# Optimization experiments

Measured on AMD Instinct MI355X. Metric: run time of the kernel, lower is better.

Reference implementation:

```python
import jax, jax.numpy as jnp
import numpy as np

N = 256
FEAT = 1024           # box_head.fc7.out_features
HID_REL = 256         # RelationProposalNetwork hidden_dim
GCN_HID = 256         # gcn_hidden
HEADS = 4
NUM_PARTS = 20
OUT = NUM_PARTS + 1
TOPK = 3
IN_GCN = FEAT + 4


def setup_inputs() -> dict:
    key = jax.random.key(0)
    ks = jax.random.split(key, 16)
    features = jax.random.normal(ks[0], (N, FEAT), jnp.float32)
    # valid pixel-space boxes (x1, y1, x2, y2) inside an 800x800 image
    xy = jax.random.uniform(ks[1], (N, 2), jnp.float32, 0.0, 700.0)
    wh = jax.random.uniform(ks[2], (N, 2), jnp.float32, 8.0, 100.0)
    boxes = jnp.concatenate([xy, xy + wh], axis=1)
    s = 0.02
    W_fc1 = jax.random.normal(ks[3], (2 * FEAT + 4, HID_REL), jnp.float32) * s
    b_fc1 = jnp.zeros((HID_REL,), jnp.float32)
    W_fc2 = jax.random.normal(ks[4], (HID_REL, 1), jnp.float32) * s
    b_fc2 = jnp.zeros((1,), jnp.float32)
    W1 = jax.random.normal(ks[5], (IN_GCN, HEADS * GCN_HID), jnp.float32) * s
    a_src1 = jax.random.normal(ks[6], (HEADS, GCN_HID), jnp.float32) * s
    a_dst1 = jax.random.normal(ks[7], (HEADS, GCN_HID), jnp.float32) * s
    b1 = jnp.zeros((HEADS * GCN_HID,), jnp.float32)
    W2 = jax.random.normal(ks[8], (HEADS * GCN_HID, OUT), jnp.float32) * s
    a_src2 = jax.random.normal(ks[9], (1, OUT), jnp.float32) * s
    a_dst2 = jax.random.normal(ks[10], (1, OUT), jnp.float32) * s
    b2 = jnp.zeros((OUT,), jnp.float32)
    return {
        "features": features, "boxes": boxes,
        "W_fc1": W_fc1, "b_fc1": b_fc1, "W_fc2": W_fc2, "b_fc2": b_fc2,
        "W1": W1, "a_src1": a_src1, "a_dst1": a_dst1, "b1": b1,
        "W2": W2, "a_src2": a_src2, "a_dst2": a_dst2, "b2": b2,
        "img_h": 800, "img_w": 800,
    }


def _gat_layer(x, W, a_src, a_dst, bias, s, t, n, heads, ch):
    # PyG GATConv: message flows edge_index[0] (s) -> edge_index[1] (t),
    # softmax over incoming edges of each target node t.
    h = (x @ W).reshape(n, heads, ch)                       # [n, H, C]
    e = jax.nn.leaky_relu(
        jnp.einsum("ehc,hc->eh", h[s], a_src)
        + jnp.einsum("ehc,hc->eh", h[t], a_dst), 0.2)        # [E, H]
    m = jnp.full((n, heads), -1e30, e.dtype).at[t].max(e)    # segment max
    p = jnp.exp(e - m[t])
    denom = jax.ops.segment_sum(p, t, num_segments=n)
    alpha = p / denom[t]                                     # [E, H]
    out = jax.ops.segment_sum(alpha[:, :, None] * h[s], t, num_segments=n)
    return out.reshape(n, heads * ch) + bias


def _forward(features, boxes, W_fc1, b_fc1, W_fc2, b_fc2,
             W1, a_src1, a_dst1, b1, W2, a_src2, a_dst2, b2, img_h, img_w):
    n = features.shape[0]
    # --- RelationProposalNetwork: dense O(N^2) pairwise MLP ---
    f1 = jnp.broadcast_to(features[:, None, :], (n, n, FEAT))
    f2 = jnp.broadcast_to(features[None, :, :], (n, n, FEAT))
    geom = jnp.abs(boxes[:, None, :] - boxes[None, :, :])    # [n, n, 4]
    pair = jnp.concatenate([f1, f2, geom], axis=-1)          # [n, n, 2052]
    hid = jax.nn.relu(pair @ W_fc1 + b_fc1)                  # [n, n, 256]
    rel = (hid @ W_fc2 + b_fc2)[..., 0]                      # [n, n]
    # --- top-k graph construction (drop first = self, as in source) ---
    idx = jax.lax.top_k(rel, TOPK + 1)[1][:, 1:]             # [n, topk]
    s_e = jnp.repeat(jnp.arange(n), TOPK)                    # edge_index[0]
    t_e = idx.reshape(-1)                                    # edge_index[1]
    loops = jnp.arange(n)                                    # GATConv add_self_loops
    s_e = jnp.concatenate([s_e, loops])
    t_e = jnp.concatenate([t_e, loops])
    # --- normalized box geometry node features ---
    scale = jnp.array([img_w, img_h, img_w, img_h], jnp.float32)
    nb = boxes / scale
    geomn = jnp.stack([nb[:, 0], nb[:, 1], nb[:, 2] - nb[:, 0], nb[:, 3] - nb[:, 1]], axis=1)
    gcn_in = jnp.concatenate([features, geomn], axis=1)      # [n, 1028]
    # --- AttentionalGCN: GAT(heads=4) -> ReLU -> GAT(heads=1) ---
    h1 = jax.nn.relu(_gat_layer(gcn_in, W1, a_src1, a_dst1, b1, s_e, t_e, n, HEADS, GCN_HID))
    logits = _gat_layer(h1, W2, a_src2, a_dst2, b2, s_e, t_e, n, 1, OUT)
    return logits


def reference(features, boxes, W_fc1, b_fc1, W_fc2, b_fc2,
              W1, a_src1, a_dst1, b1, W2, a_src2, a_dst2, b2, img_h, img_w):
    logits = _forward(features, boxes, W_fc1, b_fc1, W_fc2, b_fc2,
                      W1, a_src1, a_dst1, b1, W2, a_src2, a_dst2, b2, img_h, img_w)
    labels = jnp.argmax(logits, axis=1)
    return logits, labels
```

## Files before the change

### kernel.cpp

```cpp
#include <hip/hip_runtime.h>
#include <math.h>

#define NN 256
#define FEAT 1024
#define HIDR 256
#define HEADS 4
#define GCNH 256
#define M1 1024
#define OUTC 21
#define MAXDEG (NN + 1)
#define KC 8
#define KCH (FEAT / KC)
#define FCOLS 1536

__global__ __launch_bounds__(256) void k_big(
        const float* __restrict__ feat, const float* __restrict__ Wfc1,
        const float* __restrict__ W1, float* __restrict__ P) {
    __shared__ float fS[8][KCH];
    int rg = blockIdx.x, cg = blockIdx.y, kc = blockIdx.z;
    int tid = threadIdx.x;
    int r0 = rg * 8, k0 = kc * KCH;
    for (int x = tid; x < 8 * KCH; x += 256) {
        int r = x >> 7, kk = x & (KCH - 1);
        fS[r][kk] = feat[(size_t)(r0 + r) * FEAT + k0 + kk];
    }
    __syncthreads();
    int gc = cg * 512 + tid * 2;
    const float* pW;
    int ld;
    if (gc < 256)      { pW = Wfc1 + (size_t)k0 * HIDR + gc;                  ld = HIDR; }
    else if (gc < 512) { pW = Wfc1 + (size_t)(FEAT + k0) * HIDR + (gc - 256); ld = HIDR; }
    else               { pW = W1   + (size_t)k0 * M1 + (gc - 512);            ld = M1;   }
    float2 acc[8];
#pragma unroll
    for (int r = 0; r < 8; r++) { acc[r].x = 0.f; acc[r].y = 0.f; }
    float2 w0 = *(const float2*)(pW);
    float2 w1 = *(const float2*)(pW + ld);
    float2 w2 = *(const float2*)(pW + 2 * ld);
    float2 w3 = *(const float2*)(pW + 3 * ld);
    for (int kk = 0; kk < KCH; kk += 4) {
        pW += 4 * ld;
        float2 n0 = *(const float2*)(pW);
        float2 n1 = *(const float2*)(pW + ld);
        float2 n2 = *(const float2*)(pW + 2 * ld);
        float2 n3 = *(const float2*)(pW + 3 * ld);
#pragma unroll
        for (int r = 0; r < 8; r++) {
            float4 f = *(const float4*)&fS[r][kk];
            acc[r].x = fmaf(f.x, w0.x, acc[r].x); acc[r].y = fmaf(f.x, w0.y, acc[r].y);
            acc[r].x = fmaf(f.y, w1.x, acc[r].x); acc[r].y = fmaf(f.y, w1.y, acc[r].y);
            acc[r].x = fmaf(f.z, w2.x, acc[r].x); acc[r].y = fmaf(f.z, w2.y, acc[r].y);
            acc[r].x = fmaf(f.w, w3.x, acc[r].x); acc[r].y = fmaf(f.w, w3.y, acc[r].y);
        }
        w0 = n0; w1 = n1; w2 = n2; w3 = n3;
    }
    float* Pp = P + ((size_t)kc * NN + r0) * FCOLS + gc;
#pragma unroll
    for (int r = 0; r < 8; r++)
        *(float2*)(Pp + (size_t)r * FCOLS) = acc[r];
}

__global__ __launch_bounds__(384) void k_redfix(
        const float* __restrict__ P, const float* __restrict__ bfc1,
        const float* __restrict__ boxes, const int* __restrict__ imh,
        const int* __restrict__ imw, const float* __restrict__ W1,
        const float* __restrict__ as1, const float* __restrict__ ad1,
        float* __restrict__ A, float* __restrict__ BT4,
        float* __restrict__ hpre, float* __restrict__ es1,
        float* __restrict__ ed1, float* __restrict__ geomn) {
    __shared__ float gS[4];
    int row = blockIdx.x, tid = threadIdx.x;
    int c4 = tid * 4;
    const float* p = P + (size_t)row * FCOLS + c4;
    const size_t str = (size_t)NN * FCOLS;
    float4 t0 = *(const float4*)(p);
    float4 t1 = *(const float4*)(p + str);
    float4 t2 = *(const float4*)(p + 2 * str);
    float4 t3 = *(const float4*)(p + 3 * str);
    float4 t4 = *(const float4*)(p + 4 * str);
    float4 t5 = *(const float4*)(p + 5 * str);
    float4 t6 = *(const float4*)(p + 6 * str);
    float4 t7 = *(const float4*)(p + 7 * str);
    float4 s;
    s.x = ((t0.x + t1.x) + (t2.x + t3.x)) + ((t4.x + t5.x) + (t6.x + t7.x));
    s.y = ((t0.y + t1.y) + (t2.y + t3.y)) + ((t4.y + t5.y) + (t6.y + t7.y));
    s.z = ((t0.z + t1.z) + (t2.z + t3.z)) + ((t4.z + t5.z) + (t6.z + t7.z));
    s.w = ((t0.w + t1.w) + (t2.w + t3.w)) + ((t4.w + t5.w) + (t6.w + t7.w));
    if (tid == 0) {
        float w = (float)imw[0], h = (float)imh[0];
        float x1 = boxes[row * 4 + 0] / w, y1 = boxes[row * 4 + 1] / h;
        float x2 = boxes[row * 4 + 2] / w, y2 = boxes[row * 4 + 3] / h;
        gS[0] = x1; gS[1] = y1; gS[2] = x2 - x1; gS[3] = y2 - y1;
        geomn[row * 4 + 0] = x1;
        geomn[row * 4 + 1] = y1;
        geomn[row * 4 + 2] = x2 - x1;
        geomn[row * 4 + 3] = y2 - y1;
    }
    __syncthreads();
    if (c4 < 256) {
        float4 b = *(const float4*)(bfc1 + c4);
        s.x += b.x; s.y += b.y; s.z += b.z; s.w += b.w;
        *(float4*)(A + (size_t)row * HIDR + c4) = s;
    } else if (c4 < 512) {
        int kk = c4 - 256;
        *(float4*)(BT4 + (size_t)(kk >> 2) * (NN * 4) + row * 4) = s;
    } else {
        int ch = c4 - 512;
        float g0 = gS[0], g1 = gS[1], g2 = gS[2], g3 = gS[3];
        float4 wv;
        wv = *(const float4*)(W1 + (size_t)(FEAT + 0) * M1 + ch);
        s.x = fmaf(g0, wv.x, s.x); s.y = fmaf(g0, wv.y, s.y);
        s.z = fmaf(g0, wv.z, s.z); s.w = fmaf(g0, wv.w, s.w);
        wv = *(const float4*)(W1 + (size_t)(FEAT + 1) * M1 + ch);
        s.x = fmaf(g1, wv.x, s.x); s.y = fmaf(g1, wv.y, s.y);
        s.z = fmaf(g1, wv.z, s.z); s.w = fmaf(g1, wv.w, s.w);
        wv = *(const float4*)(W1 + (size_t)(FEAT + 2) * M1 + ch);
        s.x = fmaf(g2, wv.x, s.x); s.y = fmaf(g2, wv.y, s.y);
        s.z = fmaf(g2, wv.z, s.z); s.w = fmaf(g2, wv.w, s.w);
        wv = *(const float4*)(W1 + (size_t)(FEAT + 3) * M1 + ch);
        s.x = fmaf(g3, wv.x, s.x); s.y = fmaf(g3, wv.y, s.y);
        s.z = fmaf(g3, wv.z, s.z); s.w = fmaf(g3, wv.w, s.w);
        *(float4*)(hpre + (size_t)row * M1 + ch) = s;
        float4 a = *(const float4*)(as1 + ch);
        float4 b = *(const float4*)(ad1 + ch);
        float ps = s.x * a.x + s.y * a.y + s.z * a.z + s.w * a.w;
        float pd = s.x * b.x + s.y * b.y + s.z * b.z + s.w * b.w;
#pragma unroll
        for (int o = 32; o > 0; o >>= 1) {
            ps += __shfl_down(ps, o);
            pd += __shfl_down(pd, o);
        }
        if ((tid & 63) == 0) {
            int head = (tid - 128) >> 6;
            es1[row * 4 + head] = ps;
            ed1[row * 4 + head] = pd;
        }
    }
}

__global__ __launch_bounds__(512) void k_reltopk(
        const float* __restrict__ A, const float* __restrict__ BT4,
        const float* __restrict__ boxes, const float* __restrict__ Wfc1,
        const float* __restrict__ Wfc2, int* __restrict__ idxTop) {
    __shared__ float As[HIDR], w2s[HIDR], wg0[HIDR], wg1[HIDR], wg2[HIDR], wg3[HIDR];
    __shared__ float sval[512];
    __shared__ unsigned long long swk[8];
    __shared__ int win;
    int i = blockIdx.x, tid = threadIdx.x;
    int j = tid & 255, half = tid >> 8;
    if (tid < 256) {
        As[tid]  = A[i * HIDR + tid];
        w2s[tid] = Wfc2[tid];
        wg0[tid] = Wfc1[(size_t)(2 * FEAT + 0) * HIDR + tid];
    } else {
        int q = tid - 256;
        wg1[q] = Wfc1[(size_t)(2 * FEAT + 1) * HIDR + q];
        wg2[q] = Wfc1[(size_t)(2 * FEAT + 2) * HIDR + q];
        wg3[q] = Wfc1[(size_t)(2 * FEAT + 3) * HIDR + q];
    }
    float bi0 = boxes[i * 4 + 0], bi1 = boxes[i * 4 + 1];
    float bi2 = boxes[i * 4 + 2], bi3 = boxes[i * 4 + 3];
    float g0 = fabsf(bi0 - boxes[j * 4 + 0]);
    float g1 = fabsf(bi1 - boxes[j * 4 + 1]);
    float g2 = fabsf(bi2 - boxes[j * 4 + 2]);
    float g3 = fabsf(bi3 - boxes[j * 4 + 3]);
    __syncthreads();
    int k0 = half * 128;
    const float* pB = BT4 + (size_t)(k0 >> 2) * (NN * 4) + j * 4;
    float acc = 0.f;
    for (int kk = k0; kk < k0 + 128; kk += 4) {
        float4 a4 = *(const float4*)&As[kk];
        float4 w4 = *(const float4*)&w2s[kk];
        float4 q0 = *(const float4*)&wg0[kk];
        float4 q1 = *(const float4*)&wg1[kk];
        float4 q2 = *(const float4*)&wg2[kk];
        float4 q3 = *(const float4*)&wg3[kk];
        float4 b4 = *(const float4*)pB;
        pB += NN * 4;
        float v;
        v = a4.x + b4.x; v = fmaf(g0, q0.x, v); v = fmaf(g1, q1.x, v);
        v = fmaf(g2, q2.x, v); v = fmaf(g3, q3.x, v);
        acc = fmaf(fmaxf(v, 0.f), w4.x, acc);
        v = a4.y + b4.y; v = fmaf(g0, q0.y, v); v = fmaf(g1, q1.y, v);
        v = fmaf(g2, q2.y, v); v = fmaf(g3, q3.y, v);
        acc = fmaf(fmaxf(v, 0.f), w4.y, acc);
        v = a4.z + b4.z; v = fmaf(g0, q0.z, v); v = fmaf(g1, q1.z, v);
        v = fmaf(g2, q2.z, v); v = fmaf(g3, q3.z, v);
        acc = fmaf(fmaxf(v, 0.f), w4.z, acc);
        v = a4.w + b4.w; v = fmaf(g0, q0.w, v); v = fmaf(g1, q1.w, v);
        v = fmaf(g2, q2.w, v); v = fmaf(g3, q3.w, v);
        acc = fmaf(fmaxf(v, 0.f), w4.w, acc);
    }
    sval[tid] = acc;
    __syncthreads();
    if (tid < 256) sval[tid] = sval[tid] + sval[tid + 256];
    __syncthreads();
    for (int r = 0; r < 4; r++) {
        unsigned long long key = 0ULL;
        if (tid < 256) {
            unsigned u = __float_as_uint(sval[tid]);
            u = (u & 0x80000000u) ? ~u : (u | 0x80000000u);
            key = ((unsigned long long)u << 32) | (unsigned)(NN - 1 - tid);
        }
#pragma unroll
        for (int o = 32; o > 0; o >>= 1) {
            unsigned long long nk = __shfl_down(key, o);
            if (nk > key) key = nk;
        }
        if ((tid & 63) == 0) swk[tid >> 6] = key;
        __syncthreads();
        if (tid == 0) {
            unsigned long long m = swk[0];
#pragma unroll
            for (int q = 1; q < 8; q++) if (swk[q] > m) m = swk[q];
            int wj = NN - 1 - (int)(m & 0xFFFFFFFFu);
            win = wj;
            if (r > 0) idxTop[i * 3 + (r - 1)] = wj;
        }
        __syncthreads();
        if (tid == win) sval[tid] = -1e38f;
        __syncthreads();
    }
}

__global__ __launch_bounds__(256) void k_gat1h2(
        const float* __restrict__ idxTopF, const float* __restrict__ hpre,
        const float* __restrict__ es1, const float* __restrict__ ed1,
        const float* __restrict__ b1, const float* __restrict__ W2,
        const float* __restrict__ as2, const float* __restrict__ ad2,
        int* __restrict__ deg, int* __restrict__ inlist,
        float* __restrict__ h2, float* __restrict__ es2,
        float* __restrict__ ed2) {
    const int* idxTop = (const int*)idxTopF;
    __shared__ int pfx[NN];
    __shared__ int lst[MAXDEG];
    __shared__ int dgS;
    __shared__ float sc[MAXDEG * 4];
    __shared__ float mh[4], dh[4];
    __shared__ float sh[M1];
    __shared__ float part[12 * OUTC];
    __shared__ float h2row[OUTC];
    int t = blockIdx.x, tid = threadIdx.x;
    int f = (idxTop[tid * 3 + 0] == t) | (idxTop[tid * 3 + 1] == t)
          | (idxTop[tid * 3 + 2] == t);
    pfx[tid] = f;
    __syncthreads();
    for (int o = 1; o < NN; o <<= 1) {
        int add = (tid >= o) ? pfx[tid - o] : 0;
        __syncthreads();
        pfx[tid] += add;
        __syncthreads();
    }
    if (f) {
        lst[pfx[tid] - 1] = tid;
        inlist[t * MAXDEG + (pfx[tid] - 1)] = tid;
    }
    if (tid == NN - 1) {
        int d = pfx[NN - 1];
        lst[d] = t;
        inlist[t * MAXDEG + d] = t;
        dgS = d + 1;
        deg[t] = d + 1;
    }
    __syncthreads();
    int dg = dgS;
    for (int p = tid; p < dg * 4; p += 256) {
        int e = p >> 2, h = p & 3;
        int s = lst[e];
        float v = es1[s * 4 + h] + ed1[t * 4 + h];
        sc[p] = v >= 0.f ? v : 0.2f * v;
    }
    __syncthreads();
    if (tid < 4) {
        float m = -1e30f;
        for (int e = 0; e < dg; e++) m = fmaxf(m, sc[e * 4 + tid]);
        float s = 0.f;
        for (int e = 0; e < dg; e++) s += expf(sc[e * 4 + tid] - m);
        mh[tid] = m; dh[tid] = s;
    }
    __syncthreads();
    for (int p = tid; p < dg * 4; p += 256) {
        int h = p & 3;
        sc[p] = expf(sc[p] - mh[h]) / dh[h];
    }
    __syncthreads();
    float acc[4] = {0.f, 0.f, 0.f, 0.f};
    for (int e = 0; e < dg; e++) {
        int s = lst[e];
        const float* hs = hpre + (size_t)s * M1;
#pragma unroll
        for (int q = 0; q < 4; q++)
            acc[q] = fmaf(sc[e * 4 + q], hs[q * GCNH + tid], acc[q]);
    }
#pragma unroll
    for (int q = 0; q < 4; q++) {
        int c = q * GCNH + tid;
        sh[c] = fmaxf(acc[q] + b1[c], 0.f);
    }
    __syncthreads();
    if (tid < 252) {
        int o = tid % OUTC, p = tid / OUTC;
        float a2 = 0.f;
        for (int d = p; d < M1; d += 12)
            a2 = fmaf(sh[d], W2[d * OUTC + o], a2);
        part[p * OUTC + o] = a2;
    }
    __syncthreads();
    if (tid < OUTC) {
        float s = 0.f;
        for (int p = 0; p < 12; p++) s += part[p * OUTC + tid];
        h2[t * OUTC + tid] = s;
        h2row[tid] = s;
    }
    __syncthreads();
    if (tid == 0) {
        float s = 0.f, dd = 0.f;
        for (int k = 0; k < OUTC; k++) {
            s = fmaf(h2row[k], as2[k], s);
            dd = fmaf(h2row[k], ad2[k], dd);
        }
        es2[t] = s; ed2[t] = dd;
    }
}

__global__ __launch_bounds__(64) void k_gat2(
        const float* __restrict__ h2, const float* __restrict__ es2,
        const float* __restrict__ ed2, const int* __restrict__ deg,
        const int* __restrict__ inlist, const float* __restrict__ b2,
        float* __restrict__ out) {
    __shared__ float sc[MAXDEG];
    __shared__ float md[2];
    __shared__ float lv[OUTC];
    int t = blockIdx.x, tid = threadIdx.x;
    int dg = deg[t];
    float edt = ed2[t];
    for (int p = tid; p < dg; p += 64) {
        int s = inlist[t * MAXDEG + p];
        float v = es2[s] + edt;
        sc[p] = v >= 0.f ? v : 0.2f * v;
    }
    __syncthreads();
    if (tid == 0) {
        float m = -1e30f;
        for (int e = 0; e < dg; e++) m = fmaxf(m, sc[e]);
        float s = 0.f;
        for (int e = 0; e < dg; e++) s += expf(sc[e] - m);
        md[0] = m; md[1] = s;
    }
    __syncthreads();
    if (tid < OUTC) {
        float acc = 0.f;
        for (int e = 0; e < dg; e++) {
            int s = inlist[t * MAXDEG + e];
            float a = expf(sc[e] - md[0]) / md[1];
            acc = fmaf(a, h2[s * OUTC + tid], acc);
        }
        float v = acc + b2[tid];
        out[t * OUTC + tid] = v;
        lv[tid] = v;
    }
    __syncthreads();
    if (tid == 0) {
        int best = 0;
        float bv = lv[0];
        for (int o = 1; o < OUTC; o++)
            if (lv[o] > bv) { bv = lv[o]; best = o; }
        out[NN * OUTC + t] = (float)best;
    }
}

extern "C" void kernel_launch(void* const* d_in, const int* in_sizes, int n_in,
                              void* d_out, int out_size, void* d_ws,
                              size_t ws_size, hipStream_t stream) {
    const float* feat  = (const float*)d_in[0];
    const float* boxes = (const float*)d_in[1];
    const float* Wfc1  = (const float*)d_in[2];
    const float* bfc1  = (const float*)d_in[3];
    const float* Wfc2  = (const float*)d_in[4];
    const float* bfc2  = (const float*)d_in[5];   (void)bfc2;
    const float* W1    = (const float*)d_in[6];
    const float* as1   = (const float*)d_in[7];
    const float* ad1   = (const float*)d_in[8];
    const float* b1    = (const float*)d_in[9];
    const float* W2    = (const float*)d_in[10];
    const float* as2   = (const float*)d_in[11];
    const float* ad2   = (const float*)d_in[12];
    const float* b2    = (const float*)d_in[13];
    const int*   imh   = (const int*)d_in[14];
    const int*   imw   = (const int*)d_in[15];

    float* ws = (float*)d_ws;
    float* P     = ws;  ws += KC * NN * FCOLS;
    float* A     = ws;  ws += NN * HIDR;
    float* BT4   = ws;  ws += NN * HIDR;
    float* hpre  = ws;  ws += NN * M1;
    float* es1   = ws;  ws += NN * 4;
    float* ed1   = ws;  ws += NN * 4;
    float* h2    = ws;  ws += NN * OUTC;
    float* es2   = ws;  ws += NN;
    float* ed2   = ws;  ws += NN;
    float* geomn = ws;  ws += NN * 4;
    int* deg     = (int*)ws;
    int* inlist  = deg + NN;
    int* idxTop  = inlist + NN * MAXDEG;

    float* out = (float*)d_out;

    k_big<<<dim3(32, 3, KC), 256, 0, stream>>>(feat, Wfc1, W1, P);
    k_redfix<<<NN, 384, 0, stream>>>(P, bfc1, boxes, imh, imw, W1, as1, ad1,
                                     A, BT4, hpre, es1, ed1, geomn);
    k_reltopk<<<NN, 512, 0, stream>>>(A, BT4, boxes, Wfc1, Wfc2, idxTop);
    k_gat1h2<<<NN, 256, 0, stream>>>((const float*)idxTop, hpre, es1, ed1,
                                     b1, W2, as2, ad2, deg, inlist,
                                     h2, es2, ed2);
    k_gat2<<<NN, 64, 0, stream>>>(h2, es2, ed2, deg, inlist, b2, out);
}
```

Measured before the change: 163.2 us.

## Fuse tail kernels into one cooperative kernel with grid syncs; retile big GEMM

Merges the reduction/fixup, relation top-k, GAT layer 1 and GAT layer 2 kernels into a single cooperative kernel of 256 blocks x 512 threads. The stages are separated by grid.sync(), and the A matrix stays in shared memory instead of going through global memory. This removes three kernel launches and their gaps. The front GEMM is also retiled to 16 rows per block with 16 K-chunks, which adds more partial sums to reduce. Grid-wide barriers have their own cost, and the larger per-block register and LDS footprint could limit co-residency.

```diff
diff --git a/kernel.cpp b/kernel.cpp
--- a/kernel.cpp
+++ b/kernel.cpp
@@ -1,5 +1,8 @@
 #include <hip/hip_runtime.h>
+#include <hip/hip_cooperative_groups.h>
 #include <math.h>
+
+namespace coopg = cooperative_groups;
 
 #define NN 256
 #define FEAT 1024
@@ -9,31 +12,32 @@
 #define M1 1024
 #define OUTC 21
 #define MAXDEG (NN + 1)
-#define KC 8
+#define KC 16
 #define KCH (FEAT / KC)
+#define RB 16
 #define FCOLS 1536
 
 __global__ __launch_bounds__(256) void k_big(
         const float* __restrict__ feat, const float* __restrict__ Wfc1,
         const float* __restrict__ W1, float* __restrict__ P) {
-    __shared__ float fS[8][KCH];
-    int rg = blockIdx.x, cg = blockIdx.y, kc = blockIdx.z;
+    __shared__ float fS[RB][KCH];
+    int rg = blockIdx.x, cgy = blockIdx.y, kc = blockIdx.z;
     int tid = threadIdx.x;
-    int r0 = rg * 8, k0 = kc * KCH;
-    for (int x = tid; x < 8 * KCH; x += 256) {
-        int r = x >> 7, kk = x & (KCH - 1);
+    int r0 = rg * RB, k0 = kc * KCH;
+    for (int x = tid; x < RB * KCH; x += 256) {
+        int r = x >> 6, kk = x & (KCH - 1);
         fS[r][kk] = feat[(size_t)(r0 + r) * FEAT + k0 + kk];
     }
     __syncthreads();
-    int gc = cg * 512 + tid * 2;
+    int gc = cgy * 512 + tid * 2;
     const float* pW;
     int ld;
     if (gc < 256)      { pW = Wfc1 + (size_t)k0 * HIDR + gc;                  ld = HIDR; }
     else if (gc < 512) { pW = Wfc1 + (size_t)(FEAT + k0) * HIDR + (gc - 256); ld = HIDR; }
     else               { pW = W1   + (size_t)k0 * M1 + (gc - 512);            ld = M1;   }
-    float2 acc[8];
-#pragma unroll
-    for (int r = 0; r < 8; r++) { acc[r].x = 0.f; acc[r].y = 0.f; }
+    float2 acc[RB];
+#pragma unroll
+    for (int r = 0; r < RB; r++) { acc[r].x = 0.f; acc[r].y = 0.f; }
     float2 w0 = *(const float2*)(pW);
     float2 w1 = *(const float2*)(pW + ld);
     float2 w2 = *(const float2*)(pW + 2 * ld);
@@ -45,7 +49,7 @@
         float2 n2 = *(const float2*)(pW + 2 * ld);
         float2 n3 = *(const float2*)(pW + 3 * ld);
 #pragma unroll
-        for (int r = 0; r < 8; r++) {
+        for (int r = 0; r < RB; r++) {
             float4 f = *(const float4*)&fS[r][kk];
             acc[r].x = fmaf(f.x, w0.x, acc[r].x); acc[r].y = fmaf(f.x, w0.y, acc[r].y);
             acc[r].x = fmaf(f.y, w1.x, acc[r].x); acc[r].y = fmaf(f.y, w1.y, acc[r].y);
@@ -56,316 +60,323 @@
     }
     float* Pp = P + ((size_t)kc * NN + r0) * FCOLS + gc;
 #pragma unroll
-    for (int r = 0; r < 8; r++)
+    for (int r = 0; r < RB; r++)
         *(float2*)(Pp + (size_t)r * FCOLS) = acc[r];
 }
 
-__global__ __launch_bounds__(384) void k_redfix(
+__global__ __launch_bounds__(512) void k_tail(
         const float* __restrict__ P, const float* __restrict__ bfc1,
         const float* __restrict__ boxes, const int* __restrict__ imh,
         const int* __restrict__ imw, const float* __restrict__ W1,
         const float* __restrict__ as1, const float* __restrict__ ad1,
-        float* __restrict__ A, float* __restrict__ BT4,
+        const float* __restrict__ Wfc1, const float* __restrict__ Wfc2,
+        const float* __restrict__ b1, const float* __restrict__ W2,
+        const float* __restrict__ as2, const float* __restrict__ ad2,
+        const float* __restrict__ b2, float* __restrict__ BT4,
         float* __restrict__ hpre, float* __restrict__ es1,
-        float* __restrict__ ed1, float* __restrict__ geomn) {
+        float* __restrict__ ed1, int* __restrict__ idxTop,
+        int* __restrict__ deg, int* __restrict__ inlist,
+        float* __restrict__ h2, float* __restrict__ es2,
+        float* __restrict__ ed2, float* __restrict__ out) {
+    coopg::grid_group grid = coopg::this_grid();
     __shared__ float gS[4];
-    int row = blockIdx.x, tid = threadIdx.x;
-    int c4 = tid * 4;
-    const float* p = P + (size_t)row * FCOLS + c4;
-    const size_t str = (size_t)NN * FCOLS;
-    float4 t0 = *(const float4*)(p);
-    float4 t1 = *(const float4*)(p + str);
-    float4 t2 = *(const float4*)(p + 2 * str);
-    float4 t3 = *(const float4*)(p + 3 * str);
-    float4 t4 = *(const float4*)(p + 4 * str);
-    float4 t5 = *(const float4*)(p + 5 * str);
-    float4 t6 = *(const float4*)(p + 6 * str);
-    float4 t7 = *(const float4*)(p + 7 * str);
-    float4 s;
-    s.x = ((t0.x + t1.x) + (t2.x + t3.x)) + ((t4.x + t5.x) + (t6.x + t7.x));
-    s.y = ((t0.y + t1.y) + (t2.y + t3.y)) + ((t4.y + t5.y) + (t6.y + t7.y));
-    s.z = ((t0.z + t1.z) + (t2.z + t3.z)) + ((t4.z + t5.z) + (t6.z + t7.z));
-    s.w = ((t0.w + t1.w) + (t2.w + t3.w)) + ((t4.w + t5.w) + (t6.w + t7.w));
-    if (tid == 0) {
-        float w = (float)imw[0], h = (float)imh[0];
-        float x1 = boxes[row * 4 + 0] / w, y1 = boxes[row * 4 + 1] / h;
-        float x2 = boxes[row * 4 + 2] / w, y2 = boxes[row * 4 + 3] / h;
-        gS[0] = x1; gS[1] = y1; gS[2] = x2 - x1; gS[3] = y2 - y1;
-        geomn[row * 4 + 0] = x1;
-        geomn[row * 4 + 1] = y1;
-        geomn[row * 4 + 2] = x2 - x1;
-        geomn[row * 4 + 3] = y2 - y1;
-    }
-    __syncthreads();
-    if (c4 < 256) {
-        float4 b = *(const float4*)(bfc1 + c4);
-        s.x += b.x; s.y += b.y; s.z += b.z; s.w += b.w;
-        *(float4*)(A + (size_t)row * HIDR + c4) = s;
-    } else if (c4 < 512) {
-        int kk = c4 - 256;
-        *(float4*)(BT4 + (size_t)(kk >> 2) * (NN * 4) + row * 4) = s;
-    } else {
-        int ch = c4 - 512;
-        float g0 = gS[0], g1 = gS[1], g2 = gS[2], g3 = gS[3];
-        float4 wv;
-        wv = *(const float4*)(W1 + (size_t)(FEAT + 0) * M1 + ch);
-        s.x = fmaf(g0, wv.x, s.x); s.y = fmaf(g0, wv.y, s.y);
-        s.z = fmaf(g0, wv.z, s.z); s.w = fmaf(g0, wv.w, s.w);
-        wv = *(const float4*)(W1 + (size_t)(FEAT + 1) * M1 + ch);
-        s.x = fmaf(g1, wv.x, s.x); s.y = fmaf(g1, wv.y, s.y);
-        s.z = fmaf(g1, wv.z, s.z); s.w = fmaf(g1, wv.w, s.w);
-        wv = *(const float4*)(W1 + (size_t)(FEAT + 2) * M1 + ch);
-        s.x = fmaf(g2, wv.x, s.x); s.y = fmaf(g2, wv.y, s.y);
-        s.z = fmaf(g2, wv.z, s.z); s.w = fmaf(g2, wv.w, s.w);
-        wv = *(const float4*)(W1 + (size_t)(FEAT + 3) * M1 + ch);
-        s.x = fmaf(g3, wv.x, s.x); s.y = fmaf(g3, wv.y, s.y);
-        s.z = fmaf(g3, wv.z, s.z); s.w = fmaf(g3, wv.w, s.w);
-        *(float4*)(hpre + (size_t)row * M1 + ch) = s;
-        float4 a = *(const float4*)(as1 + ch);
-        float4 b = *(const float4*)(ad1 + ch);
-        float ps = s.x * a.x + s.y * a.y + s.z * a.z + s.w * a.w;
-        float pd = s.x * b.x + s.y * b.y + s.z * b.z + s.w * b.w;
-#pragma unroll
-        for (int o = 32; o > 0; o >>= 1) {
-            ps += __shfl_down(ps, o);
-            pd += __shfl_down(pd, o);
-        }
-        if ((tid & 63) == 0) {
-            int head = (tid - 128) >> 6;
-            es1[row * 4 + head] = ps;
-            ed1[row * 4 + head] = pd;
-        }
-    }
-}
-
-__global__ __launch_bounds__(512) void k_reltopk(
-        const float* __restrict__ A, const float* __restrict__ BT4,
-        const float* __restrict__ boxes, const float* __restrict__ Wfc1,
-        const float* __restrict__ Wfc2, int* __restrict__ idxTop) {
-    __shared__ float As[HIDR], w2s[HIDR], wg0[HIDR], wg1[HIDR], wg2[HIDR], wg3[HIDR];
+    __shared__ float As[HIDR], w2s[HIDR];
+    __shared__ float wg0[HIDR], wg1[HIDR], wg2[HIDR], wg3[HIDR];
     __shared__ float sval[512];
     __shared__ unsigned long long swk[8];
     __shared__ int win;
-    int i = blockIdx.x, tid = threadIdx.x;
-    int j = tid & 255, half = tid >> 8;
-    if (tid < 256) {
-        As[tid]  = A[i * HIDR + tid];
-        w2s[tid] = Wfc2[tid];
-        wg0[tid] = Wfc1[(size_t)(2 * FEAT + 0) * HIDR + tid];
-    } else {
-        int q = tid - 256;
-        wg1[q] = Wfc1[(size_t)(2 * FEAT + 1) * HIDR + q];
-        wg2[q] = Wfc1[(size_t)(2 * FEAT + 2) * HIDR + q];
-        wg3[q] = Wfc1[(size_t)(2 * FEAT + 3) * HIDR + q];
-    }
-    float bi0 = boxes[i * 4 + 0], bi1 = boxes[i * 4 + 1];
-    float bi2 = boxes[i * 4 + 2], bi3 = boxes[i * 4 + 3];
-    float g0 = fabsf(bi0 - boxes[j * 4 + 0]);
-    float g1 = fabsf(bi1 - boxes[j * 4 + 1]);
-    float g2 = fabsf(bi2 - boxes[j * 4 + 2]);
-    float g3 = fabsf(bi3 - boxes[j * 4 + 3]);
-    __syncthreads();
-    int k0 = half * 128;
-    const float* pB = BT4 + (size_t)(k0 >> 2) * (NN * 4) + j * 4;
-    float acc = 0.f;
-    for (int kk = k0; kk < k0 + 128; kk += 4) {
-        float4 a4 = *(const float4*)&As[kk];
-        float4 w4 = *(const float4*)&w2s[kk];
-        float4 q0 = *(const float4*)&wg0[kk];
-        float4 q1 = *(const float4*)&wg1[kk];
-        float4 q2 = *(const float4*)&wg2[kk];
-        float4 q3 = *(const float4*)&wg3[kk];
-        float4 b4 = *(const float4*)pB;
-        pB += NN * 4;
-        float v;
-        v = a4.x + b4.x; v = fmaf(g0, q0.x, v); v = fmaf(g1, q1.x, v);
-        v = fmaf(g2, q2.x, v); v = fmaf(g3, q3.x, v);
-        acc = fmaf(fmaxf(v, 0.f), w4.x, acc);
-        v = a4.y + b4.y; v = fmaf(g0, q0.y, v); v = fmaf(g1, q1.y, v);
-        v = fmaf(g2, q2.y, v); v = fmaf(g3, q3.y, v);
-        acc = fmaf(fmaxf(v, 0.f), w4.y, acc);
-        v = a4.z + b4.z; v = fmaf(g0, q0.z, v); v = fmaf(g1, q1.z, v);
-        v = fmaf(g2, q2.z, v); v = fmaf(g3, q3.z, v);
-        acc = fmaf(fmaxf(v, 0.f), w4.z, acc);
-        v = a4.w + b4.w; v = fmaf(g0, q0.w, v); v = fmaf(g1, q1.w, v);
-        v = fmaf(g2, q2.w, v); v = fmaf(g3, q3.w, v);
-        acc = fmaf(fmaxf(v, 0.f), w4.w, acc);
-    }
-    sval[tid] = acc;
-    __syncthreads();
-    if (tid < 256) sval[tid] = sval[tid] + sval[tid + 256];
-    __syncthreads();
-    for (int r = 0; r < 4; r++) {
-        unsigned long long key = 0ULL;
-        if (tid < 256) {
-            unsigned u = __float_as_uint(sval[tid]);
-            u = (u & 0x80000000u) ? ~u : (u | 0x80000000u);
-            key = ((unsigned long long)u << 32) | (unsigned)(NN - 1 - tid);
-        }
-#pragma unroll
-        for (int o = 32; o > 0; o >>= 1) {
-            unsigned long long nk = __shfl_down(key, o);
-            if (nk > key) key = nk;
-        }
-        if ((tid & 63) == 0) swk[tid >> 6] = key;
-        __syncthreads();
-        if (tid == 0) {
-            unsigned long long m = swk[0];
-#pragma unroll
-            for (int q = 1; q < 8; q++) if (swk[q] > m) m = swk[q];
-            int wj = NN - 1 - (int)(m & 0xFFFFFFFFu);
-            win = wj;
-            if (r > 0) idxTop[i * 3 + (r - 1)] = wj;
-        }
-        __syncthreads();
-        if (tid == win) sval[tid] = -1e38f;
-        __syncthreads();
-    }
-}
-
-__global__ __launch_bounds__(256) void k_gat1h2(
-        const float* __restrict__ idxTopF, const float* __restrict__ hpre,
-        const float* __restrict__ es1, const float* __restrict__ ed1,
-        const float* __restrict__ b1, const float* __restrict__ W2,
-        const float* __restrict__ as2, const float* __restrict__ ad2,
-        int* __restrict__ deg, int* __restrict__ inlist,
-        float* __restrict__ h2, float* __restrict__ es2,
-        float* __restrict__ ed2) {
-    const int* idxTop = (const int*)idxTopF;
-    __shared__ int pfx[NN];
+    __shared__ int pfxS[NN];
     __shared__ int lst[MAXDEG];
     __shared__ int dgS;
     __shared__ float sc[MAXDEG * 4];
     __shared__ float mh[4], dh[4];
-    __shared__ float sh[M1];
+    __shared__ float shh[M1];
     __shared__ float part[12 * OUTC];
     __shared__ float h2row[OUTC];
-    int t = blockIdx.x, tid = threadIdx.x;
-    int f = (idxTop[tid * 3 + 0] == t) | (idxTop[tid * 3 + 1] == t)
-          | (idxTop[tid * 3 + 2] == t);
-    pfx[tid] = f;
-    __syncthreads();
-    for (int o = 1; o < NN; o <<= 1) {
-        int add = (tid >= o) ? pfx[tid - o] : 0;
-        __syncthreads();
-        pfx[tid] += add;
-        __syncthreads();
-    }
-    if (f) {
-        lst[pfx[tid] - 1] = tid;
-        inlist[t * MAXDEG + (pfx[tid] - 1)] = tid;
-    }
-    if (tid == NN - 1) {
-        int d = pfx[NN - 1];
-        lst[d] = t;
-        inlist[t * MAXDEG + d] = t;
-        dgS = d + 1;
-        deg[t] = d + 1;
-    }
-    __syncthreads();
-    int dg = dgS;
-    for (int p = tid; p < dg * 4; p += 256) {
-        int e = p >> 2, h = p & 3;
-        int s = lst[e];
-        float v = es1[s * 4 + h] + ed1[t * 4 + h];
-        sc[p] = v >= 0.f ? v : 0.2f * v;
-    }
-    __syncthreads();
-    if (tid < 4) {
-        float m = -1e30f;
-        for (int e = 0; e < dg; e++) m = fmaxf(m, sc[e * 4 + tid]);
-        float s = 0.f;
-        for (int e = 0; e < dg; e++) s += expf(sc[e * 4 + tid] - m);
-        mh[tid] = m; dh[tid] = s;
-    }
-    __syncthreads();
-    for (int p = tid; p < dg * 4; p += 256) {
-        int h = p & 3;
-        sc[p] = expf(sc[p] - mh[h]) / dh[h];
-    }
-    __syncthreads();
-    float acc[4] = {0.f, 0.f, 0.f, 0.f};
-    for (int e = 0; e < dg; e++) {
-        int s = lst[e];
-        const float* hs = hpre + (size_t)s * M1;
-#pragma unroll
-        for (int q = 0; q < 4; q++)
-            acc[q] = fmaf(sc[e * 4 + q], hs[q * GCNH + tid], acc[q]);
-    }
-#pragma unroll
-    for (int q = 0; q < 4; q++) {
-        int c = q * GCNH + tid;
-        sh[c] = fmaxf(acc[q] + b1[c], 0.f);
-    }
-    __syncthreads();
-    if (tid < 252) {
-        int o = tid % OUTC, p = tid / OUTC;
-        float a2 = 0.f;
-        for (int d = p; d < M1; d += 12)
-            a2 = fmaf(sh[d], W2[d * OUTC + o], a2);
-        part[p * OUTC + o] = a2;
-    }
-    __syncthreads();
-    if (tid < OUTC) {
-        float s = 0.f;
-        for (int p = 0; p < 12; p++) s += part[p * OUTC + tid];
-        h2[t * OUTC + tid] = s;
-        h2row[tid] = s;
-    }
-    __syncthreads();
-    if (tid == 0) {
-        float s = 0.f, dd = 0.f;
-        for (int k = 0; k < OUTC; k++) {
-            s = fmaf(h2row[k], as2[k], s);
-            dd = fmaf(h2row[k], ad2[k], dd);
-        }
-        es2[t] = s; ed2[t] = dd;
-    }
-}
-
-__global__ __launch_bounds__(64) void k_gat2(
-        const float* __restrict__ h2, const float* __restrict__ es2,
-        const float* __restrict__ ed2, const int* __restrict__ deg,
-        const int* __restrict__ inlist, const float* __restrict__ b2,
-        float* __restrict__ out) {
-    __shared__ float sc[MAXDEG];
+    __shared__ float sc2[MAXDEG];
     __shared__ float md[2];
     __shared__ float lv[OUTC];
-    int t = blockIdx.x, tid = threadIdx.x;
-    int dg = deg[t];
-    float edt = ed2[t];
-    for (int p = tid; p < dg; p += 64) {
-        int s = inlist[t * MAXDEG + p];
-        float v = es2[s] + edt;
-        sc[p] = v >= 0.f ? v : 0.2f * v;
+
+    const int b = blockIdx.x;
+    const int tid = threadIdx.x;
+
+    if (tid == 0) {
+        float w = (float)imw[0], h = (float)imh[0];
+        float x1 = boxes[b * 4 + 0] / w, y1 = boxes[b * 4 + 1] / h;
+        float x2 = boxes[b * 4 + 2] / w, y2 = boxes[b * 4 + 3] / h;
+        gS[0] = x1; gS[1] = y1; gS[2] = x2 - x1; gS[3] = y2 - y1;
     }
     __syncthreads();
-    if (tid == 0) {
-        float m = -1e30f;
-        for (int e = 0; e < dg; e++) m = fmaxf(m, sc[e]);
-        float s = 0.f;
-        for (int e = 0; e < dg; e++) s += expf(sc[e] - m);
-        md[0] = m; md[1] = s;
-    }
-    __syncthreads();
-    if (tid < OUTC) {
+    if (tid < 384) {
+        int c4 = tid * 4;
+        const float* p = P + (size_t)b * FCOLS + c4;
+        const size_t str = (size_t)NN * FCOLS;
+        float4 a0 = *(const float4*)(p);
+        float4 a1 = *(const float4*)(p + str);
+        float4 a2 = *(const float4*)(p + 2 * str);
+        float4 a3 = *(const float4*)(p + 3 * str);
+#pragma unroll
+        for (int q = 4; q < KC; q += 4) {
+            float4 t0 = *(const float4*)(p + (size_t)q * str);
+            float4 t1 = *(const float4*)(p + (size_t)(q + 1) * str);
+            float4 t2 = *(const float4*)(p + (size_t)(q + 2) * str);
+            float4 t3 = *(const float4*)(p + (size_t)(q + 3) * str);
+            a0.x += t0.x; a0.y += t0.y; a0.z += t0.z; a0.w += t0.w;
+            a1.x += t1.x; a1.y += t1.y; a1.z += t1.z; a1.w += t1.w;
+            a2.x += t2.x; a2.y += t2.y; a2.z += t2.z; a2.w += t2.w;
+            a3.x += t3.x; a3.y += t3.y; a3.z += t3.z; a3.w += t3.w;
+        }
+        float4 s;
+        s.x = (a0.x + a1.x) + (a2.x + a3.x);
+        s.y = (a0.y + a1.y) + (a2.y + a3.y);
+        s.z = (a0.z + a1.z) + (a2.z + a3.z);
+        s.w = (a0.w + a1.w) + (a2.w + a3.w);
+        if (c4 < 256) {
+            float4 bb = *(const float4*)(bfc1 + c4);
+            As[c4 + 0] = s.x + bb.x;
+            As[c4 + 1] = s.y + bb.y;
+            As[c4 + 2] = s.z + bb.z;
+            As[c4 + 3] = s.w + bb.w;
+        } else if (c4 < 512) {
+            int kk = c4 - 256;
+            *(float4*)(BT4 + (size_t)(kk >> 2) * (NN * 4) + b * 4) = s;
+        } else {
+            int ch = c4 - 512;
+            float g0 = gS[0], g1 = gS[1], g2 = gS[2], g3 = gS[3];
+            float4 wv;
+            wv = *(const float4*)(W1 + (size_t)(FEAT + 0) * M1 + ch);
+            s.x = fmaf(g0, wv.x, s.x); s.y = fmaf(g0, wv.y, s.y);
+            s.z = fmaf(g0, wv.z, s.z); s.w = fmaf(g0, wv.w, s.w);
+            wv = *(const float4*)(W1 + (size_t)(FEAT + 1) * M1 + ch);
+            s.x = fmaf(g1, wv.x, s.x); s.y = fmaf(g1, wv.y, s.y);
+            s.z = fmaf(g1, wv.z, s.z); s.w = fmaf(g1, wv.w, s.w);
+            wv = *(const float4*)(W1 + (size_t)(FEAT + 2) * M1 + ch);
+            s.x = fmaf(g2, wv.x, s.x); s.y = fmaf(g2, wv.y, s.y);
+            s.z = fmaf(g2, wv.z, s.z); s.w = fmaf(g2, wv.w, s.w);
+            wv = *(const float4*)(W1 + (size_t)(FEAT + 3) * M1 + ch);
+            s.x = fmaf(g3, wv.x, s.x); s.y = fmaf(g3, wv.y, s.y);
+            s.z = fmaf(g3, wv.z, s.z); s.w = fmaf(g3, wv.w, s.w);
+            *(float4*)(hpre + (size_t)b * M1 + ch) = s;
+            float4 av = *(const float4*)(as1 + ch);
+            float4 dv = *(const float4*)(ad1 + ch);
+            float ps = s.x * av.x + s.y * av.y + s.z * av.z + s.w * av.w;
+            float pd = s.x * dv.x + s.y * dv.y + s.z * dv.z + s.w * dv.w;
+#pragma unroll
+            for (int o = 32; o > 0; o >>= 1) {
+                ps += __shfl_down(ps, o);
+                pd += __shfl_down(pd, o);
+            }
+            if ((tid & 63) == 0) {
+                int head = (tid - 128) >> 6;
+                es1[b * 4 + head] = ps;
+                ed1[b * 4 + head] = pd;
+            }
+        }
+    }
+    grid.sync();
+
+    {
+        int j = tid & 255, half = tid >> 8;
+        if (tid < 256) {
+            w2s[tid] = Wfc2[tid];
+            wg0[tid] = Wfc1[(size_t)(2 * FEAT + 0) * HIDR + tid];
+        } else {
+            int q = tid - 256;
+            wg1[q] = Wfc1[(size_t)(2 * FEAT + 1) * HIDR + q];
+            wg2[q] = Wfc1[(size_t)(2 * FEAT + 2) * HIDR + q];
+            wg3[q] = Wfc1[(size_t)(2 * FEAT + 3) * HIDR + q];
+        }
+        float bi0 = boxes[b * 4 + 0], bi1 = boxes[b * 4 + 1];
+        float bi2 = boxes[b * 4 + 2], bi3 = boxes[b * 4 + 3];
+        float g0 = fabsf(bi0 - boxes[j * 4 + 0]);
+        float g1 = fabsf(bi1 - boxes[j * 4 + 1]);
+        float g2 = fabsf(bi2 - boxes[j * 4 + 2]);
+        float g3 = fabsf(bi3 - boxes[j * 4 + 3]);
+        __syncthreads();
+        int k0 = half * 128;
+        const float* pB = BT4 + (size_t)(k0 >> 2) * (NN * 4) + j * 4;
         float acc = 0.f;
-        for (int e = 0; e < dg; e++) {
-            int s = inlist[t * MAXDEG + e];
-            float a = expf(sc[e] - md[0]) / md[1];
-            acc = fmaf(a, h2[s * OUTC + tid], acc);
-        }
-        float v = acc + b2[tid];
-        out[t * OUTC + tid] = v;
-        lv[tid] = v;
-    }
-    __syncthreads();
-    if (tid == 0) {
-        int best = 0;
-        float bv = lv[0];
-        for (int o = 1; o < OUTC; o++)
-            if (lv[o] > bv) { bv = lv[o]; best = o; }
-        out[NN * OUTC + t] = (float)best;
+        for (int kk = k0; kk < k0 + 128; kk += 4) {
+            float4 a4 = *(const float4*)&As[kk];
+            float4 w4 = *(const float4*)&w2s[kk];
+            float4 q0 = *(const float4*)&wg0[kk];
+            float4 q1 = *(const float4*)&wg1[kk];
+            float4 q2 = *(const float4*)&wg2[kk];
+            float4 q3 = *(const float4*)&wg3[kk];
+            float4 b4 = *(const float4*)pB;
+            pB += NN * 4;
+            float v;
+            v = a4.x + b4.x; v = fmaf(g0, q0.x, v); v = fmaf(g1, q1.x, v);
+            v = fmaf(g2, q2.x, v); v = fmaf(g3, q3.x, v);
+            acc = fmaf(fmaxf(v, 0.f), w4.x, acc);
+            v = a4.y + b4.y; v = fmaf(g0, q0.y, v); v = fmaf(g1, q1.y, v);
+            v = fmaf(g2, q2.y, v); v = fmaf(g3, q3.y, v);
+            acc = fmaf(fmaxf(v, 0.f), w4.y, acc);
+            v = a4.z + b4.z; v = fmaf(g0, q0.z, v); v = fmaf(g1, q1.z, v);
+            v = fmaf(g2, q2.z, v); v = fmaf(g3, q3.z, v);
+            acc = fmaf(fmaxf(v, 0.f), w4.z, acc);
+            v = a4.w + b4.w; v = fmaf(g0, q0.w, v); v = fmaf(g1, q1.w, v);
+            v = fmaf(g2, q2.w, v); v = fmaf(g3, q3.w, v);
+            acc = fmaf(fmaxf(v, 0.f), w4.w, acc);
+        }
+        sval[tid] = acc;
+        __syncthreads();
+        if (tid < 256) sval[tid] = sval[tid] + sval[tid + 256];
+        __syncthreads();
+        for (int r = 0; r < 4; r++) {
+            unsigned long long key = 0ULL;
+            if (tid < 256) {
+                unsigned u = __float_as_uint(sval[tid]);
+                u = (u & 0x80000000u) ? ~u : (u | 0x80000000u);
+                key = ((unsigned long long)u << 32) | (unsigned)(NN - 1 - tid);
+            }
+#pragma unroll
+            for (int o = 32; o > 0; o >>= 1) {
+                unsigned long long nk = __shfl_down(key, o);
+                if (nk > key) key = nk;
+            }
+            if ((tid & 63) == 0) swk[tid >> 6] = key;
+            __syncthreads();
+            if (tid == 0) {
+                unsigned long long m = swk[0];
+#pragma unroll
+                for (int q = 1; q < 8; q++) if (swk[q] > m) m = swk[q];
+                int wj = NN - 1 - (int)(m & 0xFFFFFFFFu);
+                win = wj;
+                if (r > 0) idxTop[b * 3 + (r - 1)] = wj;
+            }
+            __syncthreads();
+            if (tid == win) sval[tid] = -1e38f;
+            __syncthreads();
+        }
+    }
+    grid.sync();
+
+    {
+        int f = 0;
+        if (tid < NN) {
+            f = (idxTop[tid * 3 + 0] == b) | (idxTop[tid * 3 + 1] == b)
+              | (idxTop[tid * 3 + 2] == b);
+            pfxS[tid] = f;
+        }
+        __syncthreads();
+        for (int o = 1; o < NN; o <<= 1) {
+            int add = (tid >= o && tid < NN) ? pfxS[tid - o] : 0;
+            __syncthreads();
+            if (tid < NN) pfxS[tid] += add;
+            __syncthreads();
+        }
+        if (tid < NN && f) {
+            lst[pfxS[tid] - 1] = tid;
+            inlist[b * MAXDEG + (pfxS[tid] - 1)] = tid;
+        }
+        if (tid == NN - 1) {
+            int d = pfxS[NN - 1];
+            lst[d] = b;
+            inlist[b * MAXDEG + d] = b;
+            dgS = d + 1;
+            deg[b] = d + 1;
+        }
+        __syncthreads();
+        int dg = dgS;
+        for (int p = tid; p < dg * 4; p += 512) {
+            int e = p >> 2, h = p & 3;
+            int s = lst[e];
+            float v = es1[s * 4 + h] + ed1[b * 4 + h];
+            sc[p] = v >= 0.f ? v : 0.2f * v;
+        }
+        __syncthreads();
+        if (tid < 4) {
+            float m = -1e30f;
+            for (int e = 0; e < dg; e++) m = fmaxf(m, sc[e * 4 + tid]);
+            float s = 0.f;
+            for (int e = 0; e < dg; e++) s += expf(sc[e * 4 + tid] - m);
+            mh[tid] = m; dh[tid] = s;
+        }
+        __syncthreads();
+        for (int p = tid; p < dg * 4; p += 512) {
+            int h = p & 3;
+            sc[p] = expf(sc[p] - mh[h]) / dh[h];
+        }
+        __syncthreads();
+        if (tid < 256) {
+            float acc4[4] = {0.f, 0.f, 0.f, 0.f};
+            for (int e = 0; e < dg; e++) {
+                int s = lst[e];
+                const float* hs = hpre + (size_t)s * M1;
+#pragma unroll
+                for (int q = 0; q < 4; q++)
+                    acc4[q] = fmaf(sc[e * 4 + q], hs[q * GCNH + tid], acc4[q]);
+            }
+#pragma unroll
+            for (int q = 0; q < 4; q++) {
+                int c = q * GCNH + tid;
+                shh[c] = fmaxf(acc4[q] + b1[c], 0.f);
+            }
+        }
+        __syncthreads();
+        if (tid < 252) {
+            int o = tid % OUTC, p = tid / OUTC;
+            float a2 = 0.f;
+            for (int d = p; d < M1; d += 12)
+                a2 = fmaf(shh[d], W2[d * OUTC + o], a2);
+            part[p * OUTC + o] = a2;
+        }
+        __syncthreads();
+        if (tid < OUTC) {
+            float s = 0.f;
+            for (int p = 0; p < 12; p++) s += part[p * OUTC + tid];
+            h2[b * OUTC + tid] = s;
+            h2row[tid] = s;
+        }
+        __syncthreads();
+        if (tid == 0) {
+            float s = 0.f, dd = 0.f;
+            for (int k = 0; k < OUTC; k++) {
+                s = fmaf(h2row[k], as2[k], s);
+                dd = fmaf(h2row[k], ad2[k], dd);
+            }
+            es2[b] = s; ed2[b] = dd;
+        }
+    }
+    grid.sync();
+
+    {
+        int dg = deg[b];
+        float edt = ed2[b];
+        for (int p = tid; p < dg; p += 512) {
+            int s = inlist[b * MAXDEG + p];
+            float v = es2[s] + edt;
+            sc2[p] = v >= 0.f ? v : 0.2f * v;
+        }
+        __syncthreads();
+        if (tid == 0) {
+            float m = -1e30f;
+            for (int e = 0; e < dg; e++) m = fmaxf(m, sc2[e]);
+            float s = 0.f;
+            for (int e = 0; e < dg; e++) s += expf(sc2[e] - m);
+            md[0] = m; md[1] = s;
+        }
+        __syncthreads();
+        if (tid < OUTC) {
+            float acc = 0.f;
+            for (int e = 0; e < dg; e++) {
+                int s = inlist[b * MAXDEG + e];
+                float a = expf(sc2[e] - md[0]) / md[1];
+                acc = fmaf(a, h2[s * OUTC + tid], acc);
+            }
+            float v = acc + b2[tid];
+            out[b * OUTC + tid] = v;
+            lv[tid] = v;
+        }
+        __syncthreads();
+        if (tid == 0) {
+            int best = 0;
+            float bv = lv[0];
+            for (int o = 1; o < OUTC; o++)
+                if (lv[o] > bv) { bv = lv[o]; best = o; }
+            out[NN * OUTC + b] = (float)best;
+        }
     }
 }
 
@@ -391,7 +402,6 @@
 
     float* ws = (float*)d_ws;
     float* P     = ws;  ws += KC * NN * FCOLS;
-    float* A     = ws;  ws += NN * HIDR;
     float* BT4   = ws;  ws += NN * HIDR;
     float* hpre  = ws;  ws += NN * M1;
     float* es1   = ws;  ws += NN * 4;
@@ -399,19 +409,22 @@
     float* h2    = ws;  ws += NN * OUTC;
     float* es2   = ws;  ws += NN;
     float* ed2   = ws;  ws += NN;
-    float* geomn = ws;  ws += NN * 4;
     int* deg     = (int*)ws;
     int* inlist  = deg + NN;
     int* idxTop  = inlist + NN * MAXDEG;
 
     float* out = (float*)d_out;
 
-    k_big<<<dim3(32, 3, KC), 256, 0, stream>>>(feat, Wfc1, W1, P);
-    k_redfix<<<NN, 384, 0, stream>>>(P, bfc1, boxes, imh, imw, W1, as1, ad1,
-                                     A, BT4, hpre, es1, ed1, geomn);
-    k_reltopk<<<NN, 512, 0, stream>>>(A, BT4, boxes, Wfc1, Wfc2, idxTop);
-    k_gat1h2<<<NN, 256, 0, stream>>>((const float*)idxTop, hpre, es1, ed1,
-                                     b1, W2, as2, ad2, deg, inlist,
-                                     h2, es2, ed2);
-    k_gat2<<<NN, 64, 0, stream>>>(h2, es2, ed2, deg, inlist, b2, out);
+    k_big<<<dim3(NN / RB, 3, KC), 256, 0, stream>>>(feat, Wfc1, W1, P);
+
+    void* args[] = {
+        (void*)&P,   (void*)&bfc1, (void*)&boxes, (void*)&imh, (void*)&imw,
+        (void*)&W1,  (void*)&as1,  (void*)&ad1,   (void*)&Wfc1,
+        (void*)&Wfc2,(void*)&b1,   (void*)&W2,    (void*)&as2, (void*)&ad2,
+        (void*)&b2,  (void*)&BT4,  (void*)&hpre,  (void*)&es1, (void*)&ed1,
+        (void*)&idxTop, (void*)&deg, (void*)&inlist,
+        (void*)&h2,  (void*)&es2,  (void*)&ed2,   (void*)&out
+    };
+    hipLaunchCooperativeKernel(reinterpret_cast<void*>(k_tail),
+                               dim3(NN), dim3(512), args, 0, stream);
 }
```

Result: slower. 253.9 us (+55.6%).
